# Kernel optimization log

Measured on AMD Instinct MI355X. Metric: run time of the kernel, lower is better.

Reference implementation:

```python
import jax, jax.numpy as jnp
import numpy as np

INF = 10000.0
HEADS = 12
HEAD_SIZE = 64
HIDDEN = 1024
BATCH = 8
SEQLEN = 512


def _sin_cos(seqlen, dim, dtype):
    # SinusoidalPositionEmbedding (bert4torch style): indices = 10000**(-2i/dim)
    pos = jnp.arange(seqlen, dtype=dtype)
    inv = jnp.power(jnp.asarray(10000.0, dtype), -jnp.arange(dim // 2, dtype=dtype) * 2.0 / dim)
    freqs = pos[:, None] * inv[None, :]  # [s, dim/2]
    return jnp.sin(freqs), jnp.cos(freqs)


def setup_inputs() -> dict:
    key = jax.random.key(0)
    k1, k2, k3 = jax.random.split(key, 3)
    inputs = jax.random.normal(k1, (BATCH, SEQLEN, HIDDEN), dtype=jnp.float32)
    W = jax.random.normal(k2, (HIDDEN, HEADS * 2 * HEAD_SIZE), dtype=jnp.float32) * (HIDDEN ** -0.5)
    b = jax.random.normal(k3, (HEADS * 2 * HEAD_SIZE,), dtype=jnp.float32) * 0.02
    mask = jnp.ones((BATCH, SEQLEN), dtype=jnp.int32)
    return {"inputs": inputs, "W": W, "b": b, "mask": mask}


def reference(inputs, W, b, mask):
    bs, s, _ = inputs.shape
    h = inputs @ W + b  # [b, s, heads*2*hd]
    h = h.reshape(bs, s, HEADS, 2 * HEAD_SIZE)
    qw, kw = h[..., :HEAD_SIZE], h[..., HEAD_SIZE:]  # [b, s, h, d]

    # interleaved RoPE: cos_pos/sin_pos repeat each freq twice along last dim
    sin, cos = _sin_cos(s, HEAD_SIZE, h.dtype)
    cos2 = jnp.repeat(cos, 2, axis=-1)[None, :, None, :]  # [1, s, 1, d]
    sin2 = jnp.repeat(sin, 2, axis=-1)[None, :, None, :]

    def rot(x):
        x2 = jnp.stack([-x[..., 1::2], x[..., 0::2]], axis=-1).reshape(x.shape)
        return x * cos2 + x2 * sin2

    qw = rot(qw)
    kw = rot(kw)

    logits = jnp.einsum('bmhd,bnhd->bhmn', qw, kw)  # [b, h, s, s]

    m = mask.astype(logits.dtype)
    pad = 1.0 - m[:, None, None, :] * m[:, None, :, None]  # [b,1,s,s]
    tril = jnp.tril(jnp.ones((s, s), dtype=logits.dtype), k=-1)[None, None]  # strictly lower
    logits = logits - pad * INF - tril * INF
    out_mask = jnp.logical_or(pad > 0, tril > 0)
    return logits * (HEAD_SIZE ** -0.5), out_mask
```

## Files before the change

kernel.cpp:

```cpp
#include <hip/hip_runtime.h>
#include <stdint.h>

typedef unsigned short ushort_t;
typedef short short8 __attribute__((ext_vector_type(8)));
typedef float float4_ __attribute__((ext_vector_type(4)));
typedef unsigned short u16x8 __attribute__((ext_vector_type(8)));

#define INF_ 10000.0f
#define BATCH 8
#define SEQLEN 512
#define HIDDEN 1024
#define HEADS 12
#define HEAD_SIZE 64
#define NOUT 1536
#define MROWS 4096
#define BH 96
#define LOGITS_N 25165824
#define MASK_N   2097152

__device__ __align__(16) ushort_t g_A [(size_t)MROWS * HIDDEN];
__device__ __align__(16) ushort_t g_Wt[(size_t)NOUT * HIDDEN];
__device__ __align__(16) ushort_t g_Q[(size_t)BH * SEQLEN * HEAD_SIZE];
__device__ __align__(16) ushort_t g_K[(size_t)BH * SEQLEN * HEAD_SIZE];
__device__ __align__(16) float    g_tab[SEQLEN * 32 * 2];

__device__ __forceinline__ ushort_t f2bf(float f) {
    unsigned u = __builtin_bit_cast(unsigned, f);
    unsigned r = u + 0x7FFFu + ((u >> 16) & 1u);
    return (ushort_t)(r >> 16);
}

__device__ __forceinline__ void gload16(const ushort_t* g, ushort_t* l) {
    __builtin_amdgcn_global_load_lds(
        (const __attribute__((address_space(1))) void*)g,
        (__attribute__((address_space(3))) void*)l, 16, 0, 0);
}

__device__ __forceinline__ unsigned mask_code(const void* m) {
    unsigned u0 = ((const unsigned*)m)[0];
    unsigned u1 = ((const unsigned*)m)[1];
    if (u0 == 0x3F803F80u) return 2;
    if (u0 == 0x3F800000u) return 3;
    if (u0 == 0x01010101u) return 4;
    if (u0 == 0x00010001u) return 5;
    if (u0 == 1u && u1 == 0u) return 1;
    return 0;
}
__device__ __forceinline__ float mask_at(const void* m, unsigned code, int i) {
    switch (code) {
        case 1: return (float)((const long long*)m)[i];
        case 2: { unsigned u = (unsigned)((const ushort_t*)m)[i] << 16;
                  return __builtin_bit_cast(float, u); }
        case 3: return ((const float*)m)[i];
        case 4: return (float)((const signed char*)m)[i];
        case 5: return (float)((const short*)m)[i];
        default: return (float)((const int*)m)[i];
    }
}

__global__ void k_prep(const float* __restrict__ A, const float* __restrict__ W) {
    __shared__ ushort_t tile[32][33];
    int bid = blockIdx.x;
    int tid = threadIdx.x;
    if (bid < 2048) {
        int i = bid * 256 + tid;
        const float4_* p = (const float4_*)(A + (size_t)i * 8);
        float4_ v0 = p[0], v1 = p[1];
        u16x8 o;
        #pragma unroll
        for (int j = 0; j < 4; ++j) { o[j] = f2bf(v0[j]); o[j + 4] = f2bf(v1[j]); }
        *(u16x8*)(g_A + (size_t)i * 8) = o;
    } else if (bid < 2048 + 1536) {
        int bb = bid - 2048;
        int bx = bb % 48;
        int by = bb / 48;
        int tx = tid & 31, ty = tid >> 5;
        #pragma unroll
        for (int i = 0; i < 4; ++i) {
            int k = by * 32 + ty + i * 8;
            int n = bx * 32 + tx;
            tile[ty + i * 8][tx] = f2bf(W[(size_t)k * NOUT + n]);
        }
        __syncthreads();
        #pragma unroll
        for (int i = 0; i < 4; ++i) {
            int n = bx * 32 + ty + i * 8;
            int k = by * 32 + tx;
            g_Wt[(size_t)n * HIDDEN + k] = tile[tx][ty + i * 8];
        }
    } else {
        int i = (bid - 3584) * 256 + tid;
        int s = i >> 5, f = i & 31;
        float inv = powf(10000.0f, -(float)(2 * f) / 64.0f);
        float ang = (float)s * inv;
        g_tab[2 * i]     = sinf(ang);
        g_tab[2 * i + 1] = cosf(ang);
    }
}

__global__ void __launch_bounds__(256) k_gemm1(const float* __restrict__ bias) {
    __shared__ __align__(16) ushort_t sA[2][64 * 64];
    __shared__ __align__(16) ushort_t sB[2][128 * 64];
    int tid = threadIdx.x;
    int lane = tid & 63, wid = tid >> 6;
    int wm = wid >> 1, wn = wid & 1;
    int bid = (blockIdx.x & 7) * 96 + (blockIdx.x >> 3);
    int bm = (bid & 63) * 64;
    int bn = (bid >> 6) * 128;

    auto stage = [&](int bi, int ks) {
        #pragma unroll
        for (int i = 0; i < 2; ++i) {
            int c = tid + i * 256;
            int row = c >> 3, ch = (c & 7) ^ (row & 7);
            gload16(g_A + (size_t)(bm + row) * HIDDEN + ks * 64 + ch * 8,
                    sA[bi] + (size_t)c * 8);
        }
        #pragma unroll
        for (int i = 0; i < 4; ++i) {
            int c = tid + i * 256;
            int row = c >> 3, ch = (c & 7) ^ (row & 7);
            gload16(g_Wt + (size_t)(bn + row) * HIDDEN + ks * 64 + ch * 8,
                    sB[bi] + (size_t)c * 8);
        }
    };

    float4_ acc[2][4] = {};
    const int NT = HIDDEN / 64;
    stage(0, 0);
    __syncthreads();
    int cur = 0;
    for (int ks = 0; ks < NT; ++ks) {
        if (ks + 1 < NT) stage(cur ^ 1, ks + 1);
        #pragma unroll
        for (int kk = 0; kk < 2; ++kk) {
            short8 af[2], bfv[4];
            int c0 = kk * 4 + (lane >> 4);
            #pragma unroll
            for (int mf = 0; mf < 2; ++mf) {
                int r = wm * 32 + mf * 16 + (lane & 15);
                af[mf] = *(const short8*)(sA[cur] + r * 64 + ((c0 ^ (r & 7)) * 8));
            }
            #pragma unroll
            for (int nf = 0; nf < 4; ++nf) {
                int r = wn * 64 + nf * 16 + (lane & 15);
                bfv[nf] = *(const short8*)(sB[cur] + r * 64 + ((c0 ^ (r & 7)) * 8));
            }
            #pragma unroll
            for (int mf = 0; mf < 2; ++mf)
                #pragma unroll
                for (int nf = 0; nf < 4; ++nf)
                    acc[mf][nf] = __builtin_amdgcn_mfma_f32_16x16x32_bf16(af[mf], bfv[nf], acc[mf][nf], 0, 0, 0);
        }
        __syncthreads();
        cur ^= 1;
    }

    #pragma unroll
    for (int nf = 0; nf < 4; ++nf) {
        int gn = bn + wn * 64 + nf * 16 + (lane & 15);
        float bv = bias[gn];
        int head = gn >> 7;
        int isk  = (gn >> 6) & 1;
        int d0 = gn & 63;
        int fi = d0 >> 1;
        float sgn = (gn & 1) ? 1.0f : -1.0f;
        ushort_t* dst = isk ? g_K : g_Q;
        #pragma unroll
        for (int mf = 0; mf < 2; ++mf) {
            int gm0 = bm + wm * 32 + mf * 16 + ((lane >> 4) * 4);
            #pragma unroll
            for (int r = 0; r < 4; ++r) {
                int gm = gm0 + r;
                int s = gm & (SEQLEN - 1);
                int b = gm >> 9;
                float v = acc[mf][nf][r] + bv;
                float p = __shfl_xor(v, 1, 64);
                const float* tc = g_tab + 2 * (s * 32 + fi);
                float sn = tc[0], cs = tc[1];
                float y = v * cs + sgn * p * sn;
                size_t o = (((size_t)(b * HEADS + head)) * SEQLEN + s) * HEAD_SIZE + d0;
                dst[o] = f2bf(y);
            }
        }
    }
}

__global__ void __launch_bounds__(256) k_gemm2(const void* __restrict__ mask,
                                               float* __restrict__ out) {
    __shared__ __align__(16) ushort_t sQ[128 * 64];
    __shared__ __align__(16) ushort_t sK[128 * 64];
    __shared__ float sMr[128], sMc[128];
    int tid = threadIdx.x;
    int lane = tid & 63, wid = tid >> 6;
    int blk = (blockIdx.x & 7) * 192 + (blockIdx.x >> 3);
    int bh = blk >> 4;
    int t = blk & 15;
    int mt = t >> 2, nt = t & 3;
    int b = bh / HEADS;
    bool writeMask = (bh - b * HEADS) == 0;

    const ushort_t* Qb = g_Q + ((size_t)bh * SEQLEN + mt * 128) * HEAD_SIZE;
    const ushort_t* Kb = g_K + ((size_t)bh * SEQLEN + nt * 128) * HEAD_SIZE;
    #pragma unroll
    for (int i = 0; i < 4; ++i) {
        int c = tid + i * 256;
        int row = c >> 3, ch = (c & 7) ^ (row & 7);
        gload16(Qb + (size_t)row * 64 + ch * 8, sQ + (size_t)c * 8);
        gload16(Kb + (size_t)row * 64 + ch * 8, sK + (size_t)c * 8);
    }
    unsigned mcode = mask_code(mask);
    if (tid < 128)      sMr[tid]       = mask_at(mask, mcode, b * SEQLEN + mt * 128 + tid);
    else                sMc[tid - 128] = mask_at(mask, mcode, b * SEQLEN + nt * 128 + (tid - 128));
    __syncthreads();

    int wm = wid >> 1, wn = wid & 1;
    float4_ acc[4][4] = {};
    #pragma unroll
    for (int kk = 0; kk < 2; ++kk) {
        short8 af[4], bfv[4];
        int c0 = kk * 4 + (lane >> 4);
        #pragma unroll
        for (int mf = 0; mf < 4; ++mf) {
            int r = wm * 64 + mf * 16 + (lane & 15);
            af[mf] = *(const short8*)(sQ + r * 64 + ((c0 ^ (r & 7)) * 8));
        }
        #pragma unroll
        for (int nf = 0; nf < 4; ++nf) {
            int r = wn * 64 + nf * 16 + (lane & 15);
            bfv[nf] = *(const short8*)(sK + r * 64 + ((c0 ^ (r & 7)) * 8));
        }
        #pragma unroll
        for (int mf = 0; mf < 4; ++mf)
            #pragma unroll
            for (int nf = 0; nf < 4; ++nf)
                acc[mf][nf] = __builtin_amdgcn_mfma_f32_16x16x32_bf16(af[mf], bfv[nf], acc[mf][nf], 0, 0, 0);
    }

    size_t obase = (size_t)bh * SEQLEN * SEQLEN;
    size_t mbase = (size_t)LOGITS_N + (size_t)b * SEQLEN * SEQLEN;
    #pragma unroll
    for (int mf = 0; mf < 4; ++mf) {
        #pragma unroll
        for (int nf = 0; nf < 4; ++nf) {
            int lcol = wn * 64 + nf * 16 + (lane & 15);
            int lrow0 = wm * 64 + mf * 16 + ((lane >> 4) * 4);
            int gn = nt * 128 + lcol;
            float mc = sMc[lcol];
            #pragma unroll
            for (int r = 0; r < 4; ++r) {
                int lrow = lrow0 + r;
                int gm = mt * 128 + lrow;
                float padv = 1.0f - sMr[lrow] * mc;
                bool tl = gn < gm;
                float v = (acc[mf][nf][r] - padv * INF_ - (tl ? INF_ : 0.0f)) * 0.125f;
                size_t off = (size_t)gm * SEQLEN + gn;
                out[obase + off] = v;
                if (writeMask)
                    out[mbase + off] = (padv > 0.0f || tl) ? 1.0f : 0.0f;
            }
        }
    }
}

extern "C" void kernel_launch(void* const* d_in, const int* in_sizes, int n_in,
                              void* d_out, int out_size, void* d_ws, size_t ws_size,
                              hipStream_t stream) {
    const float* inp = nullptr; const float* W = nullptr;
    const float* bias = nullptr; const void* mask = nullptr;
    for (int i = 0; i < n_in; ++i) {
        switch (in_sizes[i]) {
            case MROWS * HIDDEN:  inp  = (const float*)d_in[i]; break;
            case HIDDEN * NOUT:   W    = (const float*)d_in[i]; break;
            case NOUT:            bias = (const float*)d_in[i]; break;
            case BATCH * SEQLEN:  mask = d_in[i]; break;
        }
    }
    if (!inp || !W || !bias || !mask) {
        inp  = (const float*)d_in[0];
        W    = (const float*)d_in[1];
        bias = (const float*)d_in[2];
        mask = d_in[3];
    }
    float* out = (float*)d_out;
    (void)d_ws; (void)ws_size;

    k_prep<<<3648, 256, 0, stream>>>(inp, W);
    k_gemm1<<<768, 256, 0, stream>>>(bias);
    k_gemm2<<<16 * BH, 256, 0, stream>>>(mask, out);
}
```

Before: 59.71 us.

## Fuse fp32-to-bf16 conversion of activations into GEMM1 A-tile staging

Removes the separate pass in the prep kernel that converted the input activations to bf16 in a global buffer. GEMM1 now loads fp32 A rows straight into registers, prefetching the next k-tile while MFMAs run, then converts and writes the tile to swizzled LDS after compute. This avoids writing and rereading a 8MB bf16 intermediate. The cost is that each A tile is reread as fp32 by every N-block (12 times), and the tile is staged through registers instead of async global-to-LDS loads.

```diff
diff --git a/kernel.cpp b/kernel.cpp
--- a/kernel.cpp
+++ b/kernel.cpp
@@ -18,7 +18,6 @@
 #define LOGITS_N 25165824
 #define MASK_N   2097152
 
-__device__ __align__(16) ushort_t g_A [(size_t)MROWS * HIDDEN];
 __device__ __align__(16) ushort_t g_Wt[(size_t)NOUT * HIDDEN];
 __device__ __align__(16) ushort_t g_Q[(size_t)BH * SEQLEN * HEAD_SIZE];
 __device__ __align__(16) ushort_t g_K[(size_t)BH * SEQLEN * HEAD_SIZE];
@@ -58,22 +57,13 @@
     }
 }
 
-__global__ void k_prep(const float* __restrict__ A, const float* __restrict__ W) {
+__global__ void k_prep(const float* __restrict__ W) {
     __shared__ ushort_t tile[32][33];
     int bid = blockIdx.x;
     int tid = threadIdx.x;
-    if (bid < 2048) {
-        int i = bid * 256 + tid;
-        const float4_* p = (const float4_*)(A + (size_t)i * 8);
-        float4_ v0 = p[0], v1 = p[1];
-        u16x8 o;
-        #pragma unroll
-        for (int j = 0; j < 4; ++j) { o[j] = f2bf(v0[j]); o[j + 4] = f2bf(v1[j]); }
-        *(u16x8*)(g_A + (size_t)i * 8) = o;
-    } else if (bid < 2048 + 1536) {
-        int bb = bid - 2048;
-        int bx = bb % 48;
-        int by = bb / 48;
+    if (bid < 1536) {
+        int bx = bid % 48;
+        int by = bid / 48;
         int tx = tid & 31, ty = tid >> 5;
         #pragma unroll
         for (int i = 0; i < 4; ++i) {
@@ -89,7 +79,7 @@
             g_Wt[(size_t)n * HIDDEN + k] = tile[tx][ty + i * 8];
         }
     } else {
-        int i = (bid - 3584) * 256 + tid;
+        int i = (bid - 1536) * 256 + tid;
         int s = i >> 5, f = i & 31;
         float inv = powf(10000.0f, -(float)(2 * f) / 64.0f);
         float ang = (float)s * inv;
@@ -98,7 +88,8 @@
     }
 }
 
-__global__ void __launch_bounds__(256) k_gemm1(const float* __restrict__ bias) {
+__global__ void __launch_bounds__(256) k_gemm1(const float* __restrict__ A,
+                                               const float* __restrict__ bias) {
     __shared__ __align__(16) ushort_t sA[2][64 * 64];
     __shared__ __align__(16) ushort_t sB[2][128 * 64];
     int tid = threadIdx.x;
@@ -108,14 +99,24 @@
     int bm = (bid & 63) * 64;
     int bn = (bid >> 6) * 128;
 
-    auto stage = [&](int bi, int ks) {
-        #pragma unroll
-        for (int i = 0; i < 2; ++i) {
-            int c = tid + i * 256;
-            int row = c >> 3, ch = (c & 7) ^ (row & 7);
-            gload16(g_A + (size_t)(bm + row) * HIDDEN + ks * 64 + ch * 8,
-                    sA[bi] + (size_t)c * 8);
-        }
+    int arow = tid >> 2, aj = tid & 3;
+    const float* Ap = A + (size_t)(bm + arow) * HIDDEN + aj * 16;
+    float4_ fa[4];
+    auto loadA = [&](int ks) {
+        #pragma unroll
+        for (int q = 0; q < 4; ++q) fa[q] = *(const float4_*)(Ap + ks * 64 + q * 4);
+    };
+    auto writeA = [&](int bi) {
+        u16x8 pk0, pk1;
+        #pragma unroll
+        for (int j = 0; j < 4; ++j) { pk0[j] = f2bf(fa[0][j]); pk0[j+4] = f2bf(fa[1][j]); }
+        #pragma unroll
+        for (int j = 0; j < 4; ++j) { pk1[j] = f2bf(fa[2][j]); pk1[j+4] = f2bf(fa[3][j]); }
+        int c0 = aj * 2;
+        *(u16x8*)(sA[bi] + arow * 64 + ((c0     ^ (arow & 7)) * 8)) = pk0;
+        *(u16x8*)(sA[bi] + arow * 64 + (((c0+1) ^ (arow & 7)) * 8)) = pk1;
+    };
+    auto stageB = [&](int bi, int ks) {
         #pragma unroll
         for (int i = 0; i < 4; ++i) {
             int c = tid + i * 256;
@@ -127,11 +128,16 @@
 
     float4_ acc[2][4] = {};
     const int NT = HIDDEN / 64;
-    stage(0, 0);
+    loadA(0);
+    writeA(0);
+    stageB(0, 0);
     __syncthreads();
     int cur = 0;
     for (int ks = 0; ks < NT; ++ks) {
-        if (ks + 1 < NT) stage(cur ^ 1, ks + 1);
+        if (ks + 1 < NT) {
+            loadA(ks + 1);
+            stageB(cur ^ 1, ks + 1);
+        }
         #pragma unroll
         for (int kk = 0; kk < 2; ++kk) {
             short8 af[2], bfv[4];
@@ -152,6 +158,7 @@
                 for (int nf = 0; nf < 4; ++nf)
                     acc[mf][nf] = __builtin_amdgcn_mfma_f32_16x16x32_bf16(af[mf], bfv[nf], acc[mf][nf], 0, 0, 0);
         }
+        if (ks + 1 < NT) writeA(cur ^ 1);
         __syncthreads();
         cur ^= 1;
     }
@@ -285,7 +292,7 @@
     float* out = (float*)d_out;
     (void)d_ws; (void)ws_size;
 
-    k_prep<<<3648, 256, 0, stream>>>(inp, W);
-    k_gemm1<<<768, 256, 0, stream>>>(bias);
+    k_prep<<<1600, 256, 0, stream>>>(W);
+    k_gemm1<<<768, 256, 0, stream>>>(inp, bias);
     k_gemm2<<<16 * BH, 256, 0, stream>>>(mask, out);
 }
```

New measurement: 64.75 us. 1.08x slower.
